# Kernel optimization log

Measured on AMD Instinct MI355X. Metric: run time of the kernel, lower is better.

## Reference

```python
import jax, jax.numpy as jnp
from jax import lax
import numpy as np

B, H, W, C, N = 4, 512, 512, 32, 300000
K, S, P, D = 3, 2, 1, 1  # kernel, stride, padding, dilation


def setup_inputs() -> dict:
    key = jax.random.key(0)
    kf, _ = jax.random.split(key)
    features = jax.random.normal(kf, (N, C), dtype=jnp.float32)
    # unique active coordinates (spconv requires unique sites)
    rng = np.random.default_rng(0)
    lin = rng.choice(B * H * W, size=N, replace=False)
    b = lin // (H * W)
    y = (lin // W) % H
    x = lin % W
    coors = jnp.asarray(np.stack([b, y, x], axis=1), dtype=jnp.int32)  # [N,3]
    return {"features": features, "coors": coors, "batch_size": B}


def reference(features, coors, batch_size):
    # Scatter active features onto a dense grid initialized to -inf so that
    # inputs only; outputs with no active input in window are inactive).
    neg_inf = jnp.array(-jnp.inf, dtype=features.dtype)
    dense = jnp.full((batch_size, H, W, features.shape[1]), neg_inf,
                     dtype=features.dtype)
    b, y, x = coors[:, 0], coors[:, 1], coors[:, 2]
    dense = dense.at[b, y, x].set(features)  # coords are unique
    out = lax.reduce_window(
        dense, neg_inf, lax.max,
        window_dimensions=(1, K, K, 1),
        window_strides=(1, S, S, 1),
        padding=((0, 0), (P, P), (P, P), (0, 0)),
        window_dilation=(1, D, D, 1))
    # inactive output sites -> 0 (dense view of the sparse output tensor)
    return jnp.where(jnp.isinf(out), jnp.zeros((), out.dtype), out)
```

## Files before the change

### kernel.cpp

```cpp
#include <hip/hip_runtime.h>
#include <math.h>

#define BB 4
#define HH 512
#define WW 512
#define CC 32
#define HO 256
#define WO 256

#define MAXOCC 192

__global__ void fill_zero_kernel(int4* __restrict__ g, int n4) {
    int i = blockIdx.x * blockDim.x + threadIdx.x;
    if (i < n4) g[i] = make_int4(0, 0, 0, 0);
}

__global__ void scatter_idx_kernel(const int* __restrict__ coors,
                                   int* __restrict__ grid, int n) {
    int i = blockIdx.x * blockDim.x + threadIdx.x;
    if (i >= n) return;
    int b = coors[i * 3 + 0];
    int y = coors[i * 3 + 1];
    int x = coors[i * 3 + 2];
    grid[((size_t)b * HH + y) * WW + x] = i + 1;
}

__global__ void __launch_bounds__(256)
pool_kernel(const float4* __restrict__ feat,
            const int* __restrict__ grid,
            float4* __restrict__ out) {
    int ox_base = (blockIdx.x & 7) * 32;
    int t       = (blockIdx.x >> 3) & 127;
    int b       = blockIdx.x >> 10;

    int tid = threadIdx.x;
    int cg  = tid & 7;
    int p   = tid >> 3;

    int iy0 = 4 * t - 1;
    int gx0 = 2 * ox_base - 1;
    const int* gb = grid + (size_t)b * (HH * WW);

    __shared__ int    smap[5 * 65];
    __shared__ int    srcidx[MAXOCC];
    __shared__ int    cnt;
    __shared__ float4 sfeat[MAXOCC * 8];

    if (tid == 0) cnt = 0;
    __syncthreads();

    for (int e = tid; e < 5 * 65; e += 256) {
        int r = e / 65;
        int c = e - r * 65;
        int iy = iy0 + r;
        int gx = gx0 + c;
        int v = 0;
        if ((unsigned)iy < (unsigned)HH && (unsigned)gx < (unsigned)WW)
            v = gb[iy * WW + gx];
        int m = 0;
        if (v != 0) {
            int s = atomicAdd(&cnt, 1);
            if (s < MAXOCC) { srcidx[s] = v - 1; m = s + 1; }
            else            { m = -v; }
        }
        smap[e] = m;
    }
    __syncthreads();

    int total = cnt < MAXOCC ? cnt : MAXOCC;
    for (int s = (tid >> 3); s < total; s += 32) {
        sfeat[(s << 3) + ((cg + s) & 7)] = feat[(size_t)srcidx[s] * 8 + cg];
    }
    __syncthreads();

    int lc = 2 * p;
    int mm[15];
#pragma unroll
    for (int r = 0; r < 5; ++r)
#pragma unroll
        for (int dx = 0; dx < 3; ++dx)
            mm[r * 3 + dx] = smap[r * 65 + lc + dx];

    float4 f[15];
#pragma unroll
    for (int k = 0; k < 15; ++k) {
        int s = mm[k] > 0 ? mm[k] - 1 : 0;
        f[k] = sfeat[(s << 3) + ((cg + s) & 7)];
    }
#pragma unroll
    for (int k = 0; k < 15; ++k) {
        if (mm[k] < 0) f[k] = feat[(size_t)(-mm[k] - 1) * 8 + cg];
    }

    const float NEG = -INFINITY;
    float4 acc0 = make_float4(NEG, NEG, NEG, NEG);
    float4 acc1 = make_float4(NEG, NEG, NEG, NEG);
#pragma unroll
    for (int k = 0; k < 15; ++k) {
        bool ok = mm[k] != 0;
        float fx = ok ? f[k].x : NEG;
        float fy = ok ? f[k].y : NEG;
        float fz = ok ? f[k].z : NEG;
        float fw = ok ? f[k].w : NEG;
        if (k < 9) {
            acc0.x = fmaxf(acc0.x, fx);
            acc0.y = fmaxf(acc0.y, fy);
            acc0.z = fmaxf(acc0.z, fz);
            acc0.w = fmaxf(acc0.w, fw);
        }
        if (k >= 6) {
            acc1.x = fmaxf(acc1.x, fx);
            acc1.y = fmaxf(acc1.y, fy);
            acc1.z = fmaxf(acc1.z, fz);
            acc1.w = fmaxf(acc1.w, fw);
        }
    }

    acc0.x = isinf(acc0.x) ? 0.0f : acc0.x;
    acc0.y = isinf(acc0.y) ? 0.0f : acc0.y;
    acc0.z = isinf(acc0.z) ? 0.0f : acc0.z;
    acc0.w = isinf(acc0.w) ? 0.0f : acc0.w;
    acc1.x = isinf(acc1.x) ? 0.0f : acc1.x;
    acc1.y = isinf(acc1.y) ? 0.0f : acc1.y;
    acc1.z = isinf(acc1.z) ? 0.0f : acc1.z;
    acc1.w = isinf(acc1.w) ? 0.0f : acc1.w;

    int oy0  = 2 * t;
    size_t pos0 = ((size_t)(b * HO + oy0) * WO + ox_base + p);
    out[pos0 * 8 + cg]        = acc0;
    out[(pos0 + WO) * 8 + cg] = acc1;
}

extern "C" void kernel_launch(void* const* d_in, const int* in_sizes, int n_in,
                              void* d_out, int out_size, void* d_ws, size_t ws_size,
                              hipStream_t stream) {
    const float* features = (const float*)d_in[0];
    const int*   coors    = (const int*)d_in[1];
    int n = in_sizes[0] / CC;

    int* grid = (int*)d_ws;

    {
        int n4 = (BB * HH * WW) / 4;
        int blk = 256, grd = (n4 + blk - 1) / blk;
        fill_zero_kernel<<<grd, blk, 0, stream>>>((int4*)grid, n4);
    }
    {
        int blk = 256, grd = (n + blk - 1) / blk;
        scatter_idx_kernel<<<grd, blk, 0, stream>>>(coors, grid, n);
    }
    {
        int grd = BB * (HO / 2) * (WO / 32);
        pool_kernel<<<grd, 256, 0, stream>>>((const float4*)features, grid,
                                             (float4*)d_out);
    }
}
```

Baseline: 107.5 us.

## Make pool kernel wavefront-local with ballot compaction instead of block atomics

Each of the four wavefronts in a block now handles its own 8-output-column strip. It compacts the occupied grid cells of a 5x17 halo using ballot/popcount instead of shared atomics, and stages features in a per-wave shared buffer. This removes all block-level __syncthreads and the shared atomic counter. The cost is duplicated halo loads at strip boundaries (17 columns per wave versus 65 shared). Wave-local shared memory is reused without barriers, which relies on intra-wave execution ordering.

```diff
diff --git a/kernel.cpp b/kernel.cpp
--- a/kernel.cpp
+++ b/kernel.cpp
@@ -8,7 +8,7 @@
 #define HO 256
 #define WO 256
 
-#define MAXOCC 192
+#define MAXW 56
 
 __global__ void fill_zero_kernel(int4* __restrict__ g, int n4) {
     int i = blockIdx.x * blockDim.x + threadIdx.x;
@@ -33,59 +33,76 @@
     int t       = (blockIdx.x >> 3) & 127;
     int b       = blockIdx.x >> 10;
 
-    int tid = threadIdx.x;
-    int cg  = tid & 7;
-    int p   = tid >> 3;
+    int tid  = threadIdx.x;
+    int w    = tid >> 6;
+    int lane = tid & 63;
+    int cg   = lane & 7;
+    int pl   = lane >> 3;
 
-    int iy0 = 4 * t - 1;
-    int gx0 = 2 * ox_base - 1;
+    int iy0  = 4 * t - 1;
+    int gx0w = 2 * (ox_base + w * 8) - 1;
     const int* gb = grid + (size_t)b * (HH * WW);
 
-    __shared__ int    smap[5 * 65];
-    __shared__ int    srcidx[MAXOCC];
-    __shared__ int    cnt;
-    __shared__ float4 sfeat[MAXOCC * 8];
+    __shared__ float4 sfeat[4][MAXW * 8];
+    __shared__ int    srcidx[4][MAXW];
+    __shared__ int    smap[4][5 * 17];
 
-    if (tid == 0) cnt = 0;
-    __syncthreads();
+    unsigned long long lt = (1ull << lane) - 1ull;
 
-    for (int e = tid; e < 5 * 65; e += 256) {
-        int r = e / 65;
-        int c = e - r * 65;
-        int iy = iy0 + r;
-        int gx = gx0 + c;
-        int v = 0;
-        if ((unsigned)iy < (unsigned)HH && (unsigned)gx < (unsigned)WW)
-            v = gb[iy * WW + gx];
+    int r0 = lane / 17;
+    int c0 = lane - r0 * 17;
+    int iyA = iy0 + r0, gxA = gx0w + c0;
+    int v0 = 0;
+    if ((unsigned)iyA < (unsigned)HH && (unsigned)gxA < (unsigned)WW)
+        v0 = gb[iyA * WW + gxA];
+    unsigned long long m0 = __ballot(v0 != 0);
+    int s0 = (int)__popcll(m0 & lt);
+    int base1 = (int)__popcll(m0);
+    {
         int m = 0;
-        if (v != 0) {
-            int s = atomicAdd(&cnt, 1);
-            if (s < MAXOCC) { srcidx[s] = v - 1; m = s + 1; }
-            else            { m = -v; }
+        if (v0 != 0) {
+            if (s0 < MAXW) { srcidx[w][s0] = v0 - 1; m = s0 + 1; }
+            else           { m = -v0; }
         }
-        smap[e] = m;
+        smap[w][lane] = m;
     }
-    __syncthreads();
+    int e1 = 64 + lane;
+    int r1 = e1 / 17;
+    int c1 = e1 - r1 * 17;
+    int iyB = iy0 + r1, gxB = gx0w + c1;
+    int v1 = 0;
+    if (lane < 21 && (unsigned)iyB < (unsigned)HH && (unsigned)gxB < (unsigned)WW)
+        v1 = gb[iyB * WW + gxB];
+    unsigned long long m1 = __ballot(v1 != 0);
+    int s1 = base1 + (int)__popcll(m1 & lt);
+    if (lane < 21) {
+        int m = 0;
+        if (v1 != 0) {
+            if (s1 < MAXW) { srcidx[w][s1] = v1 - 1; m = s1 + 1; }
+            else           { m = -v1; }
+        }
+        smap[w][e1] = m;
+    }
+    int cnt = base1 + (int)__popcll(m1);
+    if (cnt > MAXW) cnt = MAXW;
 
-    int total = cnt < MAXOCC ? cnt : MAXOCC;
-    for (int s = (tid >> 3); s < total; s += 32) {
-        sfeat[(s << 3) + ((cg + s) & 7)] = feat[(size_t)srcidx[s] * 8 + cg];
+    for (int s = pl; s < cnt; s += 8) {
+        sfeat[w][(s << 3) + ((cg + s) & 7)] = feat[(size_t)srcidx[w][s] * 8 + cg];
     }
-    __syncthreads();
 
-    int lc = 2 * p;
+    int lc = 2 * pl;
     int mm[15];
 #pragma unroll
     for (int r = 0; r < 5; ++r)
 #pragma unroll
         for (int dx = 0; dx < 3; ++dx)
-            mm[r * 3 + dx] = smap[r * 65 + lc + dx];
+            mm[r * 3 + dx] = smap[w][r * 17 + lc + dx];
 
     float4 f[15];
 #pragma unroll
     for (int k = 0; k < 15; ++k) {
         int s = mm[k] > 0 ? mm[k] - 1 : 0;
-        f[k] = sfeat[(s << 3) + ((cg + s) & 7)];
+        f[k] = sfeat[w][(s << 3) + ((cg + s) & 7)];
     }
 #pragma unroll
     for (int k = 0; k < 15; ++k) {
@@ -125,8 +142,8 @@
     acc1.z = isinf(acc1.z) ? 0.0f : acc1.z;
     acc1.w = isinf(acc1.w) ? 0.0f : acc1.w;
 
-    int oy0  = 2 * t;
-    size_t pos0 = ((size_t)(b * HO + oy0) * WO + ox_base + p);
+    int oy0 = 2 * t;
+    size_t pos0 = ((size_t)(b * HO + oy0) * WO + ox_base + w * 8 + pl);
     out[pos0 * 8 + cg]        = acc0;
     out[(pos0 + WO) * 8 + cg] = acc1;
 }
```

Measured after the change: 111.0 us. 1.03x slower.
